# Kernel tuning notes

Measured on AMD Instinct MI355X. Metric: run time of the kernel, lower is better.

The kernel has to match this reference:

```python
import jax, jax.numpy as jnp
import numpy as np

N = 4096            # total nodes in batched graph
B = 64              # number of graphs
NPG = 64            # nodes per graph (N = B * NPG)
HID = 64            # hidden_dim
INIT_EMB = 32       # init_emb_dim
POS = 32            # inp_dim (positional/structural feat)
KG = 100000         # num_nodes in KG embedding table
LAYER = 3           # num_gcn_layers


def setup_inputs() -> dict:
    key = jax.random.key(0)
    ks = jax.random.split(key, 10)
    # block-diagonal symmetric binary adjacency (batched graph, no self loops)
    gi = jnp.repeat(jnp.arange(B), NPG)                      # graph_indices [N]
    block = gi[:, None] == gi[None, :]
    u = jax.random.uniform(ks[0], (N, N)) < 0.1
    a = jnp.logical_and(jnp.logical_or(u, u.T), block)
    a = a.at[jnp.arange(N), jnp.arange(N)].set(False)
    adj = a.astype(jnp.float32)
    head_ids = jnp.arange(B) * NPG           # node with ndata['id']==1 per graph
    tail_ids = jnp.arange(B) * NPG + 1       # node with ndata['id']==2 per graph
    return {
        "adj": adj,
        "feat_node": jax.random.normal(ks[1], (N, POS), jnp.float32),
        "idx": jax.random.randint(ks[2], (N,), 0, KG),
        "head_ids": head_ids,
        "tail_ids": tail_ids,
        "graph_indices": gi,
        "transform": jax.random.normal(ks[3], (INIT_EMB + POS, HID), jnp.float32) * 0.05,
        "embed": jax.random.normal(ks[4], (KG, INIT_EMB), jnp.float32) * 0.05,
        "w1": jax.random.normal(ks[5], (HID, HID), jnp.float32) * 0.01,
        "b1": jnp.zeros((HID,), jnp.float32),
        "w2": jax.random.normal(ks[6], (HID, HID), jnp.float32) * 0.01,
        "b2": jnp.zeros((HID,), jnp.float32),
        "gamma1": jnp.ones((HID,), jnp.float32),
        "beta1": jnp.zeros((HID,), jnp.float32),
        "gamma2": jnp.ones((HID,), jnp.float32),
        "beta2": jnp.zeros((HID,), jnp.float32),
    }


def _att_light(query, nodefea, mask, gamma, beta):
    # Attention_light: correlation-weighted masked aggregation + LayerNorm
    cor = jnp.abs(jnp.sum(query * nodefea, axis=-1, keepdims=True))   # [N,1]
    wei = cor * nodefea                                               # [N,H]
    num_nei = jnp.sum(mask, axis=-1, keepdims=True)                   # [N,1]
    up = jax.nn.leaky_relu(mask @ wei, negative_slope=0.01)           # [N,H]
    x = up / (num_nei + 1e-8)
    mu = jnp.mean(x, axis=-1, keepdims=True)
    var = jnp.var(x, axis=-1, keepdims=True)                          # biased, as torch LN
    return gamma * (x - mu) / jnp.sqrt(var + 1e-5) + beta


def _agg(entity, neighbor, w, b):
    # Aggregator: relu((entity + neighbor) @ w + b)
    return jax.nn.relu((entity + neighbor) @ w + b)


def reference(adj, feat_node, idx, head_ids, tail_ids, graph_indices,
              transform, embed, w1, b1, w2, b2, gamma1, beta1, gamma2, beta2):
    n = adj.shape[0]
    diag = jnp.arange(n)
    # node features: cat(struct feat, KG embedding) @ transform
    init_feat = jnp.concatenate([feat_node, embed[idx]], axis=1)      # [N, INIT+POS]
    feat = init_feat @ transform                                      # [N, H]
    # per-node query features of the opposite center
    headQ = feat[head_ids][graph_indices]                             # all_c1_featQ [N,H]
    tailQ = feat[tail_ids][graph_indices]                             # all_c2_featQ [N,H]
    # adjacency powers A_0=I, A_k = binarize(A_{k-1} @ adj, diag=1)
    A = jnp.eye(n, dtype=adj.dtype)
    flat_h = [jnp.zeros((n,), adj.dtype).at[head_ids].add(1.0)]       # sum of A_0 head rows
    flat_t = [jnp.zeros((n,), adj.dtype).at[tail_ids].add(1.0)]
    for _ in range(LAYER - 1):
        M = A @ adj
        M = M.at[diag, diag].set(1.0)
        A = (M > 0).astype(adj.dtype)
        flat_h.append(jnp.sum(A[head_ids], axis=0))
        flat_t.append(jnp.sum(A[tail_ids], axis=0))
    # initial masked features (hop-0 indicator = head/tail node indicator)
    init_head = (flat_h[0] > 0).astype(feat.dtype)[:, None] * feat
    init_tail = (flat_t[0] > 0).astype(feat.dtype)[:, None] * feat
    all_feat_head = feat
    all_feat_tail = feat
    layer_all, layer_head, layer_tail = [feat], [init_head], [init_tail]
    for hop in range(LAYER - 1, -1, -1):
        f1 = flat_h[hop]                                              # [N], 0/1 per node
        f2 = flat_t[hop]
        mask1 = f1[:, None] * adj                                     # [N,N]
        mask2 = f2[:, None] * adj
        up1 = _att_light(tailQ, all_feat_head, mask1, gamma1, beta1)
        up2 = _att_light(headQ, all_feat_tail, mask2, gamma2, beta2)
        agg1 = _agg(f1[:, None] * feat, up1, w1, b1)
        agg2 = _agg(f2[:, None] * feat, up2, w2, b2)
        all_feat_head = jnp.where((f1 > 0)[:, None], agg1, all_feat_head)
        all_feat_tail = jnp.where((f2 > 0)[:, None], agg2, all_feat_tail)
        layer_all.append(all_feat_head + all_feat_tail)
        layer_head.append(all_feat_head)
        layer_tail.append(all_feat_tail)
    # cat along feature dim then view -> stack on new axis 1
    return jnp.stack(layer_all, axis=1)                               # [N, LAYER+1, H]
```

## Files before the change

kernel.cpp:

```cpp
#include <hip/hip_runtime.h>

#define LD 68
#define XP 72

typedef float f32x4 __attribute__((ext_vector_type(4)));
typedef short s16x8 __attribute__((ext_vector_type(8)));
typedef unsigned long long u64;

__device__ __forceinline__ unsigned short f2bf(float f) {
  union { float f; unsigned int u; } v; v.f = f;
  const unsigned int r = (v.u + 0x7fffu + ((v.u >> 16) & 1u)) >> 16;
  return (unsigned short)r;
}
__device__ __forceinline__ float bf2f(unsigned short h) {
  union { unsigned int u; float f; } v; v.u = ((unsigned int)h) << 16;
  return v.f;
}

__global__ __launch_bounds__(512) void lagat_kernel(
    const float* __restrict__ adj,
    const float* __restrict__ feat_node,
    const int* __restrict__ idx,
    const int* __restrict__ head_ids,
    const int* __restrict__ tail_ids,
    const float* __restrict__ transform,
    const float* __restrict__ embed,
    const float* __restrict__ w1, const float* __restrict__ b1,
    const float* __restrict__ w2, const float* __restrict__ b2,
    const float* __restrict__ gamma1, const float* __restrict__ beta1,
    const float* __restrict__ gamma2, const float* __restrict__ beta2,
    float* __restrict__ out)
{
  __shared__ __align__(16) unsigned short CSTs[2][64][XP];
  __shared__ __align__(16) float Sb[2][64][LD];
  __shared__ __align__(16) float featb[64][LD];
  __shared__ __align__(16) float Ib[64][LD];
  __shared__ __align__(16) float Wb[2][4096];
  __shared__ __align__(16) float Tb[4096];
  __shared__ __align__(16) float prm[2][3][64];
  __shared__ u64 adjbits[64];
  __shared__ u64 lev[2][3];
  __shared__ float degs[64];
  __shared__ float corr[2][64];

  const int g = blockIdx.x, tid = threadIdx.x, nb = g * 64;
  const int wv = tid >> 6, lane = tid & 63;
  const int ech = wv >> 2, eslab = (wv & 3) * 16;
  const int ln15 = lane & 15, lg = lane >> 4, lg4 = lg * 4;
  const int iNode = eslab + ln15;

  {
#pragma unroll
    for (int rr = 0; rr < 8; ++rr) {
      const int row = wv * 8 + rr;
      const u64 b = __ballot(adj[(size_t)(nb + row) * 4096 + nb + lane] != 0.0f);
      if (lane == 0) adjbits[row] = b;
    }
  }
  {
    const int r = tid >> 3, c8 = (tid & 7) * 8;
    if (c8 < 32) {
      const float4* fs = (const float4*)&feat_node[(size_t)(nb + r) * 32 + c8];
      *(float4*)&Ib[r][c8]     = fs[0];
      *(float4*)&Ib[r][c8 + 4] = fs[1];
    } else {
      const float4* es = (const float4*)&embed[(size_t)idx[nb + r] * 32 + (c8 - 32)];
      *(float4*)&Ib[r][c8]     = es[0];
      *(float4*)&Ib[r][c8 + 4] = es[1];
    }
  }
  {
    const int base = tid * 16;
    const float* src = (base < 4096) ? &w1[base] : &w2[base - 4096];
    float* dst = &Wb[0][0] + base;
#pragma unroll
    for (int u = 0; u < 4; ++u)
      *(float4*)&dst[u * 4] = *(const float4*)&src[u * 4];
  }
  {
    const int tb = tid * 8;
    *(float4*)&Tb[tb]     = *(const float4*)&transform[tb];
    *(float4*)&Tb[tb + 4] = *(const float4*)&transform[tb + 4];
  }
  if (tid < 384) {
    const int a = tid >> 6, h = tid & 63;
    const float* s6 = (a == 0) ? gamma1 : (a == 1) ? beta1 : (a == 2) ? b1
                    : (a == 3) ? gamma2 : (a == 4) ? beta2 : b2;
    prm[a / 3][a % 3][h] = s6[h];
  }
  __syncthreads();

  const int hl = head_ids[g] - nb, tl = tail_ids[g] - nb;

  if (tid < 64) {
    degs[tid] = (float)__popcll(adjbits[tid]);
  } else if (tid < 192) {
    const int c = (tid >> 6) - 1;
    const int root = c ? tl : hl;
    const u64 l0 = 1ull << root;
    const u64 l1 = l0 | adjbits[root];
    u64 cand = ((l1 >> lane) & 1ull) ? adjbits[lane] : 0ull;
#pragma unroll
    for (int m = 1; m < 64; m <<= 1) cand |= __shfl_xor(cand, m, 64);
    if (lane == 0) { lev[c][0] = l0; lev[c][1] = l1; lev[c][2] = l0 | cand; }
  }
  s16x8 wfh[8], afr[2];
  {
    const float* Wl = Wb[ech];
#pragma unroll
    for (int ct = 0; ct < 4; ++ct)
#pragma unroll
      for (int ks = 0; ks < 2; ++ks) {
        s16x8 h;
#pragma unroll
        for (int j = 0; j < 8; ++j)
          h[j] = (short)f2bf(Wl[(ks * 32 + lg * 8 + j) * 64 + ct * 16 + ln15]);
        wfh[ct * 2 + ks] = h;
      }
    const u64 abits = adjbits[iNode];
#pragma unroll
    for (int ks = 0; ks < 2; ++ks) {
      s16x8 a;
#pragma unroll
      for (int j = 0; j < 8; ++j)
        a[j] = (short)(((abits >> (ks * 32 + lg * 8 + j)) & 1ull) ? 0x3F80 : 0);
      afr[ks] = a;
    }
  }
  if (ech == 0) {
    s16x8 ihf[2], ilf[2];
#pragma unroll
    for (int ks = 0; ks < 2; ++ks) {
      const float4 i0 = *(const float4*)&Ib[iNode][ks * 32 + lg * 8];
      const float4 i1 = *(const float4*)&Ib[iNode][ks * 32 + lg * 8 + 4];
      const float iv[8] = {i0.x, i0.y, i0.z, i0.w, i1.x, i1.y, i1.z, i1.w};
      s16x8 hh, ll;
#pragma unroll
      for (int j = 0; j < 8; ++j) {
        const unsigned short h = f2bf(iv[j]);
        hh[j] = (short)h;
        ll[j] = (short)f2bf(iv[j] - bf2f(h));
      }
      ihf[ks] = hh; ilf[ks] = ll;
    }
    f32x4 facc[4] = {{0,0,0,0},{0,0,0,0},{0,0,0,0},{0,0,0,0}};
#pragma unroll
    for (int ct = 0; ct < 4; ++ct)
#pragma unroll
      for (int ks = 0; ks < 2; ++ks) {
        s16x8 th;
#pragma unroll
        for (int j = 0; j < 8; ++j)
          th[j] = (short)f2bf(Tb[(ks * 32 + lg * 8 + j) * 64 + ct * 16 + ln15]);
        facc[ct] = __builtin_amdgcn_mfma_f32_16x16x32_bf16(th, ihf[ks], facc[ct], 0, 0, 0);
        facc[ct] = __builtin_amdgcn_mfma_f32_16x16x32_bf16(th, ilf[ks], facc[ct], 0, 0, 0);
      }
#pragma unroll
    for (int ct = 0; ct < 4; ++ct)
      *(float4*)&featb[iNode][ct * 16 + lg4] =
          make_float4(facc[ct][0], facc[ct][1], facc[ct][2], facc[ct][3]);
  }
  __syncthreads();

  {
    const int ch2 = tid >> 8, t = tid & 255;
    const int j = t >> 2, q = t & 3;
    const int qr = ch2 ? hl : tl;
    float s = 0.f;
#pragma unroll
    for (int u = 0; u < 4; ++u) {
      const float4 q4 = *(const float4*)&featb[qr][q * 16 + 4 * u];
      const float4 f4 = *(const float4*)&featb[j][q * 16 + 4 * u];
      s = fmaf(q4.x, f4.x, s); s = fmaf(q4.y, f4.y, s);
      s = fmaf(q4.z, f4.z, s); s = fmaf(q4.w, f4.w, s);
    }
    s += __shfl_xor(s, 1);
    s += __shfl_xor(s, 2);
    if (q == 0) corr[ch2][j] = fabsf(s);
  }
  {
    const int r = tid >> 3, c8 = (tid & 7) * 8;
#pragma unroll
    for (int u = 0; u < 2; ++u) {
      const float4 v = *(const float4*)&featb[r][c8 + 4 * u];
      *(float4*)&Sb[0][r][c8 + 4 * u] = v;
      *(float4*)&Sb[1][r][c8 + 4 * u] = v;
      *(float4*)&out[(size_t)(nb + r) * 256 + c8 + 4 * u] = v;
    }
  }
  const float dnv = 1.f / (degs[iNode] + 1e-8f);
  f32x4 ft4[4];
#pragma unroll
  for (int ct = 0; ct < 4; ++ct) {
    const int ebase = ((ct >> 1) << 5) + lg * 8 + ((ct & 1) << 2);
    ft4[ct] = *(const f32x4*)&featb[iNode][ebase];
  }
  __syncthreads();

  {
    const int ch2 = tid >> 8, t = tid & 255;
    const int c = t >> 2, j0 = (t & 3) * 16;
    const int rho = ((c >> 5) & 1) * 32 + ((c >> 2) & 1) * 16 +
                    ((c >> 4) & 1) * 8 + ((c >> 3) & 1) * 4 + (c & 3);
#pragma unroll
    for (int half = 0; half < 2; ++half) {
      s16x8 hh;
#pragma unroll
      for (int m = 0; m < 8; ++m) {
        const int j = j0 + half * 8 + m;
        hh[m] = (short)f2bf(corr[ch2][j] * featb[j][c]);
      }
      *(s16x8*)&CSTs[ch2][rho][j0 + half * 8] = hh;
    }
  }
  __syncthreads();

  const int r8 = tid >> 3, cc8 = (tid & 7) * 8;
  const int qrowE = ech ? hl : tl;

  u64 levCh[3];
#pragma unroll
  for (int k = 0; k < 3; ++k) levCh[k] = lev[ech][k];
  f32x4 qe4[4], bias4[4];
#pragma unroll
  for (int ct = 0; ct < 4; ++ct) {
    qe4[ct] = *(const f32x4*)&featb[qrowE][ct * 16 + lg4];
    bias4[ct] = *(const f32x4*)&prm[ech][2][ct * 16 + lg4];
  }

  for (int hop = 2; hop >= 0; --hop) {
    if (hop != 2) {
      const int L = 2 - hop;
#pragma unroll
      for (int u = 0; u < 2; ++u) {
        const float4 a = *(const float4*)&Sb[0][r8][cc8 + 4 * u];
        const float4 b = *(const float4*)&Sb[1][r8][cc8 + 4 * u];
        *(float4*)&out[(size_t)(nb + r8) * 256 + (size_t)L * 64 + cc8 + 4 * u] =
            make_float4(a.x + b.x, a.y + b.y, a.z + b.z, a.w + b.w);
      }
    }

    f32x4 accB[4] = {{0,0,0,0},{0,0,0,0},{0,0,0,0},{0,0,0,0}};
#pragma unroll
    for (int ct = 0; ct < 4; ++ct)
#pragma unroll
      for (int ks = 0; ks < 2; ++ks) {
        const s16x8 ah = *(const s16x8*)&CSTs[ech][ct * 16 + ln15][ks * 32 + lg * 8];
        accB[ct] = __builtin_amdgcn_mfma_f32_16x16x32_bf16(ah, afr[ks], accB[ct], 0, 0, 0);
      }
    const float fB = (float)((levCh[hop] >> iNode) & 1ull);
    float x[4][4];
    {
      float smm = 0.f, s2m = 0.f;
#pragma unroll
      for (int ct = 0; ct < 4; ++ct)
#pragma unroll
        for (int r = 0; r < 4; ++r) {
          float z = accB[ct][r];
          z = (z > 0.f) ? z : 0.01f * z;
          z *= dnv;
          x[ct][r] = z; smm += z; s2m = fmaf(z, z, s2m);
        }
      smm += __shfl_xor(smm, 16); smm += __shfl_xor(smm, 32);
      s2m += __shfl_xor(s2m, 16); s2m += __shfl_xor(s2m, 32);
      const float mu = smm * 0.015625f;
      const float var = fmaxf(s2m * 0.015625f - mu * mu, 0.f);
      const float rstd = rsqrtf(var + 1e-5f);
#pragma unroll
      for (int ct = 0; ct < 4; ++ct) {
        const int ebase = ((ct >> 1) << 5) + lg * 8 + ((ct & 1) << 2);
        const f32x4 ga4 = *(const f32x4*)&prm[ech][0][ebase];
        const f32x4 be4 = *(const f32x4*)&prm[ech][1][ebase];
#pragma unroll
        for (int r = 0; r < 4; ++r)
          x[ct][r] = fmaf(fB, ft4[ct][r], ga4[r] * (x[ct][r] - mu) * rstd + be4[r]);
      }
    }
    s16x8 xh2[2], xl2[2];
#pragma unroll
    for (int ks = 0; ks < 2; ++ks) {
      s16x8 hh, ll;
#pragma unroll
      for (int j = 0; j < 8; ++j) {
        const float xv = x[2 * ks + (j >> 2)][j & 3];
        const unsigned short h = f2bf(xv);
        hh[j] = (short)h;
        ll[j] = (short)f2bf(xv - bf2f(h));
      }
      xh2[ks] = hh; xl2[ks] = ll;
    }
    f32x4 accE[4];
#pragma unroll
    for (int ct = 0; ct < 4; ++ct) {
      accE[ct] = bias4[ct];
#pragma unroll
      for (int ks = 0; ks < 2; ++ks) {
        accE[ct] = __builtin_amdgcn_mfma_f32_16x16x32_bf16(wfh[ct*2+ks], xh2[ks], accE[ct], 0, 0, 0);
        accE[ct] = __builtin_amdgcn_mfma_f32_16x16x32_bf16(wfh[ct*2+ks], xl2[ks], accE[ct], 0, 0, 0);
      }
    }
    float s[4][4], v = 0.f;
#pragma unroll
    for (int ct = 0; ct < 4; ++ct)
#pragma unroll
      for (int r = 0; r < 4; ++r) {
        const float sv = fmaxf(accE[ct][r], 0.f);
        s[ct][r] = sv;
        v = fmaf(qe4[ct][r], sv, v);
      }
    v += __shfl_xor(v, 16); v += __shfl_xor(v, 32);
    const float vc = fabsf(v);
    const float fE = (float)((levCh[hop] >> iNode) & 1ull);

    __syncthreads();

    if (fE != 0.f) {
#pragma unroll
      for (int ct = 0; ct < 4; ++ct) {
        *(float4*)&Sb[ech][iNode][ct * 16 + lg4] =
            make_float4(s[ct][0], s[ct][1], s[ct][2], s[ct][3]);
        if (hop) {
          const int rbase = ((ct >> 1) << 5) + ((lg & 1) << 4) +
                            ((ct & 1) << 3) + ((lg >> 1) << 2);
#pragma unroll
          for (int r = 0; r < 4; ++r)
            CSTs[ech][rbase + r][iNode] = f2bf(vc * s[ct][r]);
        }
      }
    }
    __syncthreads();
  }

  {
#pragma unroll
    for (int u = 0; u < 2; ++u) {
      const float4 a = *(const float4*)&Sb[0][r8][cc8 + 4 * u];
      const float4 b = *(const float4*)&Sb[1][r8][cc8 + 4 * u];
      *(float4*)&out[(size_t)(nb + r8) * 256 + 192 + cc8 + 4 * u] =
          make_float4(a.x + b.x, a.y + b.y, a.z + b.z, a.w + b.w);
    }
  }
}

extern "C" void kernel_launch(void* const* d_in, const int* in_sizes, int n_in,
                              void* d_out, int out_size, void* d_ws, size_t ws_size,
                              hipStream_t stream) {
  const float* adj       = (const float*)d_in[0];
  const float* feat_node = (const float*)d_in[1];
  const int*   idx       = (const int*)d_in[2];
  const int*   head_ids  = (const int*)d_in[3];
  const int*   tail_ids  = (const int*)d_in[4];
  const float* transform = (const float*)d_in[6];
  const float* embed     = (const float*)d_in[7];
  const float* w1v    = (const float*)d_in[8];
  const float* b1v    = (const float*)d_in[9];
  const float* w2v    = (const float*)d_in[10];
  const float* b2v    = (const float*)d_in[11];
  const float* gamma1 = (const float*)d_in[12];
  const float* beta1  = (const float*)d_in[13];
  const float* gamma2 = (const float*)d_in[14];
  const float* beta2  = (const float*)d_in[15];

  lagat_kernel<<<64, 512, 0, stream>>>(adj, feat_node, idx, head_ids, tail_ids,
      transform, embed, w1v, b1v, w2v, b2v, gamma1, beta1, gamma2, beta2,
      (float*)d_out);
}
```

Before: 19.49 us.

## Transpose weights in LDS and fuse correlation into CST build, dropping a barrier

Weights and transform are stored transposed in shared memory so each lane builds its bf16 MFMA fragments from two float4 reads instead of eight strided scalar loads. The separate correlation pass and the CST construction pass are merged: each wave computes the query-node dot products from registers with cross-lane shuffles and writes the scaled bf16 values straight into CSTs. This removes the corr buffer and one __syncthreads. In exchange the transposed stores at setup are scattered scalar writes that may cause LDS bank conflicts, and the CST writes are column-strided.

```diff
diff --git a/kernel.cpp b/kernel.cpp
--- a/kernel.cpp
+++ b/kernel.cpp
@@ -35,13 +35,12 @@
   __shared__ __align__(16) float Sb[2][64][LD];
   __shared__ __align__(16) float featb[64][LD];
   __shared__ __align__(16) float Ib[64][LD];
-  __shared__ __align__(16) float Wb[2][4096];
-  __shared__ __align__(16) float Tb[4096];
+  __shared__ __align__(16) float Wt[2][64][LD];
+  __shared__ __align__(16) float Tt[64][LD];
   __shared__ __align__(16) float prm[2][3][64];
   __shared__ u64 adjbits[64];
   __shared__ u64 lev[2][3];
   __shared__ float degs[64];
-  __shared__ float corr[2][64];
 
   const int g = blockIdx.x, tid = threadIdx.x, nb = g * 64;
   const int wv = tid >> 6, lane = tid & 63;
@@ -71,16 +70,30 @@
   }
   {
     const int base = tid * 16;
-    const float* src = (base < 4096) ? &w1[base] : &w2[base - 4096];
-    float* dst = &Wb[0][0] + base;
-#pragma unroll
-    for (int u = 0; u < 4; ++u)
-      *(float4*)&dst[u * 4] = *(const float4*)&src[u * 4];
-  }
-  {
-    const int tb = tid * 8;
-    *(float4*)&Tb[tb]     = *(const float4*)&transform[tb];
-    *(float4*)&Tb[tb + 4] = *(const float4*)&transform[tb + 4];
+    const int m = base >> 12, off = base & 4095;
+    const int k = off >> 6, c0 = off & 63;
+    const float* src = (m ? w2 : w1) + (size_t)k * 64 + c0;
+#pragma unroll
+    for (int u = 0; u < 4; ++u) {
+      const float4 v = *(const float4*)&src[u * 4];
+      Wt[m][c0 + 4 * u][k]     = v.x;
+      Wt[m][c0 + 4 * u + 1][k] = v.y;
+      Wt[m][c0 + 4 * u + 2][k] = v.z;
+      Wt[m][c0 + 4 * u + 3][k] = v.w;
+    }
+  }
+  {
+    const int base = tid * 8;
+    const int k = base >> 6, c0 = base & 63;
+    const float* src = transform + (size_t)k * 64 + c0;
+#pragma unroll
+    for (int u = 0; u < 2; ++u) {
+      const float4 v = *(const float4*)&src[u * 4];
+      Tt[c0 + 4 * u][k]     = v.x;
+      Tt[c0 + 4 * u + 1][k] = v.y;
+      Tt[c0 + 4 * u + 2][k] = v.z;
+      Tt[c0 + 4 * u + 3][k] = v.w;
+    }
   }
   if (tid < 384) {
     const int a = tid >> 6, h = tid & 63;
@@ -106,15 +119,17 @@
   }
   s16x8 wfh[8], afr[2];
   {
-    const float* Wl = Wb[ech];
 #pragma unroll
     for (int ct = 0; ct < 4; ++ct)
 #pragma unroll
       for (int ks = 0; ks < 2; ++ks) {
+        const float4 v0 = *(const float4*)&Wt[ech][ct * 16 + ln15][ks * 32 + lg * 8];
+        const float4 v1 = *(const float4*)&Wt[ech][ct * 16 + ln15][ks * 32 + lg * 8 + 4];
         s16x8 h;
-#pragma unroll
-        for (int j = 0; j < 8; ++j)
-          h[j] = (short)f2bf(Wl[(ks * 32 + lg * 8 + j) * 64 + ct * 16 + ln15]);
+        h[0] = (short)f2bf(v0.x); h[1] = (short)f2bf(v0.y);
+        h[2] = (short)f2bf(v0.z); h[3] = (short)f2bf(v0.w);
+        h[4] = (short)f2bf(v1.x); h[5] = (short)f2bf(v1.y);
+        h[6] = (short)f2bf(v1.z); h[7] = (short)f2bf(v1.w);
         wfh[ct * 2 + ks] = h;
       }
     const u64 abits = adjbits[iNode];
@@ -148,10 +163,13 @@
     for (int ct = 0; ct < 4; ++ct)
 #pragma unroll
       for (int ks = 0; ks < 2; ++ks) {
+        const float4 t0 = *(const float4*)&Tt[ct * 16 + ln15][ks * 32 + lg * 8];
+        const float4 t1 = *(const float4*)&Tt[ct * 16 + ln15][ks * 32 + lg * 8 + 4];
         s16x8 th;
-#pragma unroll
-        for (int j = 0; j < 8; ++j)
-          th[j] = (short)f2bf(Tb[(ks * 32 + lg * 8 + j) * 64 + ct * 16 + ln15]);
+        th[0] = (short)f2bf(t0.x); th[1] = (short)f2bf(t0.y);
+        th[2] = (short)f2bf(t0.z); th[3] = (short)f2bf(t0.w);
+        th[4] = (short)f2bf(t1.x); th[5] = (short)f2bf(t1.y);
+        th[6] = (short)f2bf(t1.z); th[7] = (short)f2bf(t1.w);
         facc[ct] = __builtin_amdgcn_mfma_f32_16x16x32_bf16(th, ihf[ks], facc[ct], 0, 0, 0);
         facc[ct] = __builtin_amdgcn_mfma_f32_16x16x32_bf16(th, ilf[ks], facc[ct], 0, 0, 0);
       }
@@ -162,22 +180,6 @@
   }
   __syncthreads();
 
-  {
-    const int ch2 = tid >> 8, t = tid & 255;
-    const int j = t >> 2, q = t & 3;
-    const int qr = ch2 ? hl : tl;
-    float s = 0.f;
-#pragma unroll
-    for (int u = 0; u < 4; ++u) {
-      const float4 q4 = *(const float4*)&featb[qr][q * 16 + 4 * u];
-      const float4 f4 = *(const float4*)&featb[j][q * 16 + 4 * u];
-      s = fmaf(q4.x, f4.x, s); s = fmaf(q4.y, f4.y, s);
-      s = fmaf(q4.z, f4.z, s); s = fmaf(q4.w, f4.w, s);
-    }
-    s += __shfl_xor(s, 1);
-    s += __shfl_xor(s, 2);
-    if (q == 0) corr[ch2][j] = fabsf(s);
-  }
   {
     const int r = tid >> 3, c8 = (tid & 7) * 8;
 #pragma unroll
@@ -189,44 +191,41 @@
     }
   }
   const float dnv = 1.f / (degs[iNode] + 1e-8f);
-  f32x4 ft4[4];
+  const int qrowE = ech ? hl : tl;
+  u64 levCh[3];
+#pragma unroll
+  for (int k = 0; k < 3; ++k) levCh[k] = lev[ech][k];
+  f32x4 ft4[4], qe4[4], bias4[4];
 #pragma unroll
   for (int ct = 0; ct < 4; ++ct) {
     const int ebase = ((ct >> 1) << 5) + lg * 8 + ((ct & 1) << 2);
     ft4[ct] = *(const f32x4*)&featb[iNode][ebase];
-  }
-  __syncthreads();
-
-  {
-    const int ch2 = tid >> 8, t = tid & 255;
-    const int c = t >> 2, j0 = (t & 3) * 16;
-    const int rho = ((c >> 5) & 1) * 32 + ((c >> 2) & 1) * 16 +
-                    ((c >> 4) & 1) * 8 + ((c >> 3) & 1) * 4 + (c & 3);
-#pragma unroll
-    for (int half = 0; half < 2; ++half) {
-      s16x8 hh;
-#pragma unroll
-      for (int m = 0; m < 8; ++m) {
-        const int j = j0 + half * 8 + m;
-        hh[m] = (short)f2bf(corr[ch2][j] * featb[j][c]);
-      }
-      *(s16x8*)&CSTs[ch2][rho][j0 + half * 8] = hh;
-    }
-  }
-  __syncthreads();
-
-  const int r8 = tid >> 3, cc8 = (tid & 7) * 8;
-  const int qrowE = ech ? hl : tl;
-
-  u64 levCh[3];
-#pragma unroll
-  for (int k = 0; k < 3; ++k) levCh[k] = lev[ech][k];
-  f32x4 qe4[4], bias4[4];
-#pragma unroll
-  for (int ct = 0; ct < 4; ++ct) {
     qe4[ct] = *(const f32x4*)&featb[qrowE][ct * 16 + lg4];
     bias4[ct] = *(const f32x4*)&prm[ech][2][ct * 16 + lg4];
   }
+  {
+    f32x4 sf4[4];
+    float v = 0.f;
+#pragma unroll
+    for (int ct = 0; ct < 4; ++ct) {
+      sf4[ct] = *(const f32x4*)&featb[iNode][ct * 16 + lg4];
+#pragma unroll
+      for (int r = 0; r < 4; ++r) v = fmaf(qe4[ct][r], sf4[ct][r], v);
+    }
+    v += __shfl_xor(v, 16); v += __shfl_xor(v, 32);
+    const float vc = fabsf(v);
+#pragma unroll
+    for (int ct = 0; ct < 4; ++ct) {
+      const int rbase = ((ct >> 1) << 5) + ((lg & 1) << 4) +
+                        ((ct & 1) << 3) + ((lg >> 1) << 2);
+#pragma unroll
+      for (int r = 0; r < 4; ++r)
+        CSTs[ech][rbase + r][iNode] = f2bf(vc * sf4[ct][r]);
+    }
+  }
+  __syncthreads();
+
+  const int r8 = tid >> 3, cc8 = (tid & 7) * 8;
 
   for (int hop = 2; hop >= 0; --hop) {
     if (hop != 2) {
```

Result: faster. 18.35 us (-5.8%).
